# Performance work log

Hardware: AMD Instinct MI355X
Metric: run time of the kernel (lower is better)

The kernel has to match this reference:

```python
import jax, jax.numpy as jnp
import numpy as np

HEADS = 4
DIM_HEAD = 32
GROUPS = 32  # min(256//4, 32)
EPS = 1e-5


def setup_inputs() -> dict:
    key = jax.random.key(0)
    ks = jax.random.split(key, 6)
    B, C, H, W = 16, 256, 64, 64
    hidden = HEADS * DIM_HEAD  # 128
    return {
        "x": jax.random.normal(ks[0], (B, C, H, W), dtype=jnp.float32),
        "gn_w": jax.random.uniform(ks[1], (C,), dtype=jnp.float32),
        "gn_b": jax.random.normal(ks[2], (C,), dtype=jnp.float32) * 0.05,
        "qkv_w": jax.random.normal(ks[3], (3 * hidden, C), dtype=jnp.float32) * 0.05,
        "qkv_b": jax.random.normal(ks[4], (3 * hidden,), dtype=jnp.float32) * 0.05,
        "out_w": jax.random.normal(ks[5], (C, hidden), dtype=jnp.float32) * 0.05,
        "out_b": jnp.zeros((C,), dtype=jnp.float32),
    }


def _forward_single(x, gn_w, gn_b, qkv_w, qkv_b, out_w, out_b):
    # x: (c, h, w)
    c, h, w = x.shape
    # GroupNorm over (channels-in-group, h, w)
    xg = x.reshape(GROUPS, c // GROUPS, h, w)
    mean = xg.mean(axis=(1, 2, 3), keepdims=True)
    var = xg.var(axis=(1, 2, 3), keepdims=True)
    xn = ((xg - mean) * jax.lax.rsqrt(var + EPS)).reshape(c, h, w)
    xn = xn * gn_w[:, None, None] + gn_b[:, None, None]
    # 1x1 conv QKV projection
    qkv = jnp.einsum('oc,chw->ohw', qkv_w, xn) + qkv_b[:, None, None]
    qkv = qkv.reshape(3, HEADS, DIM_HEAD, h * w)
    q, k, v = qkv[0], qkv[1], qkv[2]
    k = jax.nn.softmax(k, axis=-1)  # softmax over spatial
    context = jnp.einsum('hdn,hen->hde', k, v)   # (heads, d, d)
    out = jnp.einsum('hde,hdn->hen', context, q)  # (heads, d, n)
    out = out.reshape(HEADS * DIM_HEAD, h, w)
    # 1x1 conv output projection
    return jnp.einsum('oc,chw->ohw', out_w, out) + out_b[:, None, None]


def reference(x, gn_w, gn_b, qkv_w, qkv_b, out_w, out_b):
    f = lambda xi: _forward_single(xi, gn_w, gn_b, qkv_w, qkv_b, out_w, out_b)
    return jax.vmap(f)(x)
```

## Files before the change

kernel.cpp:

```cpp
#include <hip/hip_runtime.h>
#include <stdint.h>

typedef unsigned short u16;
typedef __attribute__((ext_vector_type(8))) short bf16x8;
typedef __attribute__((ext_vector_type(4))) float f32x4;

#define B_   16
#define C_   256
#define HW_  4096
#define QR_  384
#define HID_ 128

__device__ __forceinline__ float b2f(u16 u) {
  union { uint32_t i; float f; } v; v.i = ((uint32_t)u) << 16; return v.f;
}
__device__ __forceinline__ u16 f2b(float f) {
  union { float f; uint32_t i; } v; v.f = f;
  uint32_t r = (v.i + 0x7FFFu + ((v.i >> 16) & 1u)) >> 16;
  return (u16)r;
}

__global__ __launch_bounds__(256) void gn_stats_conv_kernel(
    const float* __restrict__ x, const float* __restrict__ gnw,
    const float* __restrict__ gnb, float* __restrict__ scale,
    float* __restrict__ shiftv,
    const float* __restrict__ qkvw, u16* __restrict__ cqkvw,
    u16* __restrict__ wqT, unsigned int* __restrict__ cnt,
    float* __restrict__ ctxs)
{
  if (blockIdx.x >= 512) {
    int bi = blockIdx.x - 512;
    int t = threadIdx.x;
    if (bi < 96) {
      int i = bi * 256 + t;
      float4 f = ((const float4*)qkvw)[i];
      ushort4 o;
      o.x = f2b(f.x); o.y = f2b(f.y); o.z = f2b(f.z); o.w = f2b(f.w);
      ((ushort4*)cqkvw)[i] = o;
      return;
    }
    if (bi >= 97) {
      int z = (bi - 97) * 256 + t;
      ((float4*)ctxs)[z] = make_float4(0.f, 0.f, 0.f, 0.f);
      return;
    }
    if (t < 16) cnt[t] = 0;
    __shared__ u16 tl[16][272];
    for (int j = 0; j < 8; ++j) {
      int d = j * 16 + (t >> 4);
      int cb = (t & 15) * 16;
#pragma unroll
      for (int ii = 0; ii < 16; ++ii)
        tl[t >> 4][cb + ii] = f2b(qkvw[(size_t)d * 256 + cb + ii]);
      __syncthreads();
      union { u16 v[16]; uint4 q[2]; } pk;
#pragma unroll
      for (int dd = 0; dd < 16; ++dd) pk.v[dd] = tl[dd][t];
      *(uint4*)(wqT + (size_t)t * 128 + j * 16)     = pk.q[0];
      *(uint4*)(wqT + (size_t)t * 128 + j * 16 + 8) = pk.q[1];
      __syncthreads();
    }
    return;
  }
  int b = blockIdx.x >> 5, g = blockIdx.x & 31;
  const float* p = x + ((size_t)b * C_ + g * 8) * HW_;
  int t = threadIdx.x;
  float s = 0.f, sq = 0.f;
#pragma unroll
  for (int i = 0; i < 16; ++i) {
    float4 u0 = *(const float4*)(p + t * 8 + i * 2048);
    float4 u1 = *(const float4*)(p + t * 8 + i * 2048 + 4);
    s  += u0.x + u0.y + u0.z + u0.w + u1.x + u1.y + u1.z + u1.w;
    sq += u0.x*u0.x + u0.y*u0.y + u0.z*u0.z + u0.w*u0.w
        + u1.x*u1.x + u1.y*u1.y + u1.z*u1.z + u1.w*u1.w;
  }
#pragma unroll
  for (int off = 32; off > 0; off >>= 1) {
    s  += __shfl_down(s, off);
    sq += __shfl_down(sq, off);
  }
  __shared__ float ps[4], pq[4], mr[2];
  int lane = t & 63, w = t >> 6;
  if (lane == 0) { ps[w] = s; pq[w] = sq; }
  __syncthreads();
  if (t == 0) {
    float S = ps[0] + ps[1] + ps[2] + ps[3];
    float Q = pq[0] + pq[1] + pq[2] + pq[3];
    float mean = S * (1.f / 32768.f);
    float var  = Q * (1.f / 32768.f) - mean * mean;
    mr[0] = mean; mr[1] = rsqrtf(var + 1e-5f);
  }
  __syncthreads();
  if (t < 8) {
    int c = g * 8 + t;
    float sc = gnw[c] * mr[1];
    scale[b * C_ + c]  = sc;
    shiftv[b * C_ + c] = gnb[c] - mr[0] * sc;
  }
}

__global__ __launch_bounds__(256) void gn_transpose_kernel(
    const float* __restrict__ x, u16* __restrict__ dst,
    const float* __restrict__ scale, const float* __restrict__ shiftv)
{
  int nt = blockIdx.x, ct = blockIdx.y, b = blockIdx.z;
  const float* S = x + (size_t)b * C_ * HW_;
  u16* D = dst + (size_t)b * HW_ * C_;
  __shared__ __align__(16) u16 tile[64][136];
  int t = threadIdx.x;
  int n0 = nt * 128, c0 = ct * 64;
  int r = t >> 2, seg = (t & 3) * 32;
  float sc = scale[(size_t)b * C_ + c0 + r];
  float sh = shiftv[(size_t)b * C_ + c0 + r];
#pragma unroll
  for (int i = 0; i < 4; ++i) {
    const float* rp = S + (size_t)(c0 + r) * HW_ + n0 + seg + i * 8;
    float4 u0 = *(const float4*)(rp);
    float4 u1 = *(const float4*)(rp + 4);
    float f[8] = {u0.x, u0.y, u0.z, u0.w, u1.x, u1.y, u1.z, u1.w};
    uint4 o;
    uint32_t* op = (uint32_t*)&o;
#pragma unroll
    for (int j = 0; j < 4; ++j) {
      op[j] = (uint32_t)f2b(f[2 * j] * sc + sh)
            | ((uint32_t)f2b(f[2 * j + 1] * sc + sh) << 16);
    }
    *(uint4*)&tile[r][seg + i * 8] = o;
  }
  __syncthreads();
#pragma unroll
  for (int i = 0; i < 4; ++i) {
    int m = t * 4 + i;
    int n_l = m >> 3, cg = (m & 7) * 8;
    union { u16 v[8]; uint4 q; } pk;
#pragma unroll
    for (int e = 0; e < 8; ++e) pk.v[e] = tile[cg + e][n_l];
    *(uint4*)(D + (size_t)(n0 + n_l) * C_ + c0 + cg) = pk.q;
  }
}

__global__ __launch_bounds__(512) void kv_ctx_kernel(
    const u16* __restrict__ A,
    const u16* __restrict__ Bt,
    float* __restrict__ ctx,
    float* __restrict__ sv)
{
  const int K = C_;
  int nt = blockIdx.x, b = blockIdx.y;
  const u16* Ab = A;
  const u16* Bb = Bt + (size_t)b * HW_ * C_ + (size_t)nt * 128 * K;
  __shared__ __align__(16) union {
    struct { u16 lA[256 * 64]; u16 lB[128 * 64]; } st;
    struct { u16 ek[128][136]; u16 vv[128][136]; float sred[2][128]; } ep;
    float cred[4096];
  } sm;
  int t = threadIdx.x;
  int lane = t & 63, w = t >> 6;
  int quad = lane >> 4, l16 = lane & 15;
  int wm = (w >> 1) * 64, wn = (w & 1) * 64;
  f32x4 acc[4][4];
#pragma unroll
  for (int i = 0; i < 4; ++i)
#pragma unroll
    for (int j = 0; j < 4; ++j)
#pragma unroll
      for (int r = 0; r < 4; ++r) acc[i][j][r] = 0.f;

  for (int k0 = 0; k0 < K; k0 += 64) {
    __syncthreads();
#pragma unroll
    for (int q = 0; q < 4; ++q) {
      int ch = q * 512 + t;
      int row = ch >> 3, off = (ch & 7) * 8;
      __builtin_amdgcn_global_load_lds(
          (const __attribute__((address_space(1))) void*)(Ab + (size_t)row * K + k0 + off),
          (__attribute__((address_space(3))) void*)(sm.st.lA + ch * 8), 16, 0, 0);
    }
#pragma unroll
    for (int q = 0; q < 2; ++q) {
      int ch = q * 512 + t;
      int row = ch >> 3, off = (ch & 7) * 8;
      __builtin_amdgcn_global_load_lds(
          (const __attribute__((address_space(1))) void*)(Bb + (size_t)row * K + k0 + off),
          (__attribute__((address_space(3))) void*)(sm.st.lB + ch * 8), 16, 0, 0);
    }
    __syncthreads();
    const bf16x8* A8 = (const bf16x8*)sm.st.lA;
    const bf16x8* B8 = (const bf16x8*)sm.st.lB;
#pragma unroll
    for (int kk = 0; kk < 2; ++kk) {
      bf16x8 af[4], bfr[4];
#pragma unroll
      for (int i = 0; i < 4; ++i) af[i]  = A8[(wm + i * 16 + l16) * 8 + kk * 4 + quad];
#pragma unroll
      for (int j = 0; j < 4; ++j) bfr[j] = B8[(wn + j * 16 + l16) * 8 + kk * 4 + quad];
#pragma unroll
      for (int i = 0; i < 4; ++i)
#pragma unroll
        for (int j = 0; j < 4; ++j)
          acc[i][j] = __builtin_amdgcn_mfma_f32_16x16x32_bf16(af[i], bfr[j],
                                                              acc[i][j], 0, 0, 0);
    }
  }

  __syncthreads();
  int h = w >> 1, nh = w & 1;
  if (w < 4) {
    float sl[4][4];
#pragma unroll
    for (int i = 0; i < 4; ++i)
#pragma unroll
      for (int r = 0; r < 4; ++r) sl[i][r] = 0.f;
#pragma unroll
    for (int i = 0; i < 4; ++i)
#pragma unroll
      for (int j = 0; j < 4; ++j)
#pragma unroll
        for (int r = 0; r < 4; ++r) {
          float e = __expf(acc[i][j][r]);
          sl[i][r] += e;
          sm.ep.ek[wm + i * 16 + quad * 4 + r][wn + j * 16 + l16] = f2b(e);
        }
#pragma unroll
    for (int i = 0; i < 4; ++i)
#pragma unroll
      for (int r = 0; r < 4; ++r) {
        float v = sl[i][r];
        v += __shfl_xor(v, 1);
        v += __shfl_xor(v, 2);
        v += __shfl_xor(v, 4);
        v += __shfl_xor(v, 8);
        if (l16 == 0) sm.ep.sred[nh][wm + i * 16 + quad * 4 + r] = v;
      }
  } else {
#pragma unroll
    for (int i = 0; i < 4; ++i)
#pragma unroll
      for (int j = 0; j < 4; ++j)
#pragma unroll
        for (int r = 0; r < 4; ++r)
          sm.ep.vv[wm - 128 + i * 16 + quad * 4 + r][wn + j * 16 + l16] =
              f2b(acc[i][j][r]);
  }
  __syncthreads();
  if (t < 128)
    atomicAdd(&sv[(size_t)b * 128 + t], sm.ep.sred[0][t] + sm.ep.sred[1][t]);

  f32x4 c2[2][2];
#pragma unroll
  for (int i = 0; i < 2; ++i)
#pragma unroll
    for (int j = 0; j < 2; ++j)
#pragma unroll
      for (int r = 0; r < 4; ++r) c2[i][j][r] = 0.f;
#pragma unroll
  for (int kk = 0; kk < 2; ++kk) {
    bf16x8 ae[2], be[2];
#pragma unroll
    for (int i = 0; i < 2; ++i)
      ae[i] = *(const bf16x8*)&sm.ep.ek[h * 32 + i * 16 + l16][nh * 64 + kk * 32 + quad * 8];
#pragma unroll
    for (int j = 0; j < 2; ++j)
      be[j] = *(const bf16x8*)&sm.ep.vv[h * 32 + j * 16 + l16][nh * 64 + kk * 32 + quad * 8];
#pragma unroll
    for (int i = 0; i < 2; ++i)
#pragma unroll
      for (int j = 0; j < 2; ++j)
        c2[i][j] = __builtin_amdgcn_mfma_f32_16x16x32_bf16(ae[i], be[j], c2[i][j], 0, 0, 0);
  }
  __syncthreads();
  if (nh == 0) {
#pragma unroll
    for (int i = 0; i < 2; ++i)
#pragma unroll
      for (int j = 0; j < 2; ++j)
#pragma unroll
        for (int r = 0; r < 4; ++r)
          sm.cred[h * 1024 + (i * 16 + quad * 4 + r) * 32 + j * 16 + l16] = c2[i][j][r];
  }
  __syncthreads();
  if (nh == 1) {
#pragma unroll
    for (int i = 0; i < 2; ++i)
#pragma unroll
      for (int j = 0; j < 2; ++j)
#pragma unroll
        for (int r = 0; r < 4; ++r)
          sm.cred[h * 1024 + (i * 16 + quad * 4 + r) * 32 + j * 16 + l16] += c2[i][j][r];
  }
  __syncthreads();
  float* ctxb = ctx + (size_t)b * 4096;
#pragma unroll
  for (int u = 0; u < 8; ++u)
    atomicAdd(&ctxb[t + u * 512], sm.cred[t + u * 512]);
}

__global__ __launch_bounds__(256) void foldwtot_kernel(
    const float* __restrict__ ctx, const float* __restrict__ sv,
    const float* __restrict__ outw, const float* __restrict__ qkvb,
    const u16* __restrict__ wqT, const float* __restrict__ outb,
    u16* __restrict__ wf, u16* __restrict__ wtot,
    float* __restrict__ btot, unsigned int* __restrict__ cnt)
{
  int b = blockIdx.x >> 2, h = blockIdx.x & 3;
  int t = threadIdx.x;
  __shared__ float cs[1024];
  __shared__ float sinv[32];
  __shared__ unsigned int oldc;
  __shared__ __align__(16) u16 wfl[256 * 136];
  *(float4*)&cs[t * 4] = *(const float4*)(ctx + ((size_t)b * 4 + h) * 1024 + t * 4);
  if (t < 32) sinv[t] = 1.f / sv[(size_t)b * 128 + h * 32 + t];
  __syncthreads();
  {
    int o = t;
    const float* wr = outw + (size_t)o * HID_ + h * 32;
    float wv[32];
    float cb = 0.f;
#pragma unroll
    for (int e = 0; e < 32; ++e) {
      wv[e] = wr[e];
      cb += wv[e] * qkvb[256 + h * 32 + e];
    }
    union { u16 v[32]; uint4 q[4]; } pk;
#pragma unroll
    for (int d = 0; d < 32; ++d) {
      float a = 0.f;
#pragma unroll
      for (int e = 0; e < 32; ++e) a += wv[e] * cs[d * 32 + e];
      pk.v[d] = f2b(a * sinv[d] + cb);
    }
    uint4* dp = (uint4*)(wf + ((size_t)b * C_ + o) * HID_ + h * 32);
#pragma unroll
    for (int i = 0; i < 4; ++i) dp[i] = pk.q[i];
  }

  __threadfence();
  __syncthreads();
  if (t == 0) oldc = atomicAdd(&cnt[b], 1u);
  __syncthreads();
  if (oldc != 3) return;
  __threadfence();

  const uint4* ws4 = (const uint4*)(wf + (size_t)b * C_ * HID_);
  for (int i = t; i < 4096; i += 256) {
    uint4 v = ws4[i];
    int o_ = i >> 4, off = (i & 15) * 8;
    *(uint4*)&wfl[o_ * 136 + off] = v;
  }
  __syncthreads();
  {
    float a = outb[t];
#pragma unroll
    for (int d = 0; d < 128; ++d) a += b2f(wfl[t * 136 + d]) * qkvb[d];
    btot[(size_t)b * C_ + t] = a;
  }
  int lane = t & 63, w = t >> 6;
  int quad = lane >> 4, l16 = lane & 15;
  u16* Wb = wtot + (size_t)b * C_ * C_;
  for (int j = 0; j < 16; ++j) {
    f32x4 a4[4];
#pragma unroll
    for (int i = 0; i < 4; ++i)
#pragma unroll
      for (int r = 0; r < 4; ++r) a4[i][r] = 0.f;
#pragma unroll
    for (int kk = 0; kk < 4; ++kk) {
      bf16x8 bfj = *(const bf16x8*)(wqT + (size_t)(j * 16 + l16) * 128 + kk * 32 + quad * 8);
#pragma unroll
      for (int i = 0; i < 4; ++i) {
        bf16x8 afi = *(const bf16x8*)&wfl[(w * 64 + i * 16 + l16) * 136 + kk * 32 + quad * 8];
        a4[i] = __builtin_amdgcn_mfma_f32_16x16x32_bf16(bfj, afi, a4[i], 0, 0, 0);
      }
    }
#pragma unroll
    for (int i = 0; i < 4; ++i) {
      int oo = w * 64 + i * 16 + l16;
      int c0 = j * 16 + quad * 4;
      uint2 p2;
      p2.x = (uint32_t)f2b(a4[i][0]) | ((uint32_t)f2b(a4[i][1]) << 16);
      p2.y = (uint32_t)f2b(a4[i][2]) | ((uint32_t)f2b(a4[i][3]) << 16);
      *(uint2*)(Wb + (size_t)oo * C_ + c0) = p2;
    }
  }
}

__global__ __launch_bounds__(256) void out_gemm_kernel(
    const u16* __restrict__ wtot, const u16* __restrict__ Bt,
    const float* __restrict__ btot, float* __restrict__ Cout)
{
  const int K = C_;
  int nt = blockIdx.x, mt = blockIdx.y, b = blockIdx.z;
  const u16* Ab = wtot + (size_t)b * C_ * C_ + (size_t)mt * 128 * K;
  const u16* Bb = Bt + (size_t)b * HW_ * C_ + (size_t)nt * 128 * K;
  __shared__ __align__(16) u16 lA[128 * 64];
  __shared__ __align__(16) u16 lB[128 * 64];
  int t = threadIdx.x;
  int lane = t & 63, w = t >> 6;
  int quad = lane >> 4, l16 = lane & 15;
  int wm = (w >> 1) * 64, wn = (w & 1) * 64;
  f32x4 acc[4][4];
#pragma unroll
  for (int j = 0; j < 4; ++j)
#pragma unroll
    for (int i = 0; i < 4; ++i)
#pragma unroll
      for (int r = 0; r < 4; ++r) acc[j][i][r] = 0.f;

  for (int k0 = 0; k0 < K; k0 += 64) {
    __syncthreads();
#pragma unroll
    for (int q = 0; q < 4; ++q) {
      int ch = q * 256 + t;
      int row = ch >> 3, off = (ch & 7) * 8;
      __builtin_amdgcn_global_load_lds(
          (const __attribute__((address_space(1))) void*)(Ab + (size_t)row * K + k0 + off),
          (__attribute__((address_space(3))) void*)(lA + ch * 8), 16, 0, 0);
      __builtin_amdgcn_global_load_lds(
          (const __attribute__((address_space(1))) void*)(Bb + (size_t)row * K + k0 + off),
          (__attribute__((address_space(3))) void*)(lB + ch * 8), 16, 0, 0);
    }
    __syncthreads();
    const bf16x8* A8 = (const bf16x8*)lA;
    const bf16x8* B8 = (const bf16x8*)lB;
#pragma unroll
    for (int kk = 0; kk < 2; ++kk) {
      bf16x8 af[4], bfr[4];
#pragma unroll
      for (int i = 0; i < 4; ++i) af[i]  = A8[(wm + i * 16 + l16) * 8 + kk * 4 + quad];
#pragma unroll
      for (int j = 0; j < 4; ++j) bfr[j] = B8[(wn + j * 16 + l16) * 8 + kk * 4 + quad];
#pragma unroll
      for (int j = 0; j < 4; ++j)
#pragma unroll
        for (int i = 0; i < 4; ++i)
          acc[j][i] = __builtin_amdgcn_mfma_f32_16x16x32_bf16(bfr[j], af[i],
                                                              acc[j][i], 0, 0, 0);
    }
  }
#pragma unroll
  for (int i = 0; i < 4; ++i) {
    int o = mt * 128 + wm + i * 16 + l16;
    float bo = btot[(size_t)b * C_ + o];
    size_t rowbase = (size_t)b * C_ * HW_ + (size_t)o * HW_;
#pragma unroll
    for (int j = 0; j < 4; ++j) {
      int n0 = nt * 128 + wn + j * 16 + quad * 4;
      float4 v = make_float4(acc[j][i][0] + bo, acc[j][i][1] + bo,
                             acc[j][i][2] + bo, acc[j][i][3] + bo);
      *(float4*)(Cout + rowbase + n0) = v;
    }
  }
}

extern "C" void kernel_launch(void* const* d_in, const int* in_sizes, int n_in,
                              void* d_out, int out_size, void* d_ws, size_t ws_size,
                              hipStream_t stream)
{
  const float* x    = (const float*)d_in[0];
  const float* gnw  = (const float*)d_in[1];
  const float* gnb  = (const float*)d_in[2];
  const float* qkvw = (const float*)d_in[3];
  const float* qkvb = (const float*)d_in[4];
  const float* outw = (const float*)d_in[5];
  const float* outb = (const float*)d_in[6];

  char* p = (char*)d_ws;
  float* scale  = (float*)p;            p += (size_t)B_ * C_ * 4;
  float* shiftv = (float*)p;            p += (size_t)B_ * C_ * 4;
  u16* cqkvw = (u16*)p;                 p += (size_t)QR_ * C_ * 2;
  u16* wqT   = (u16*)p;                 p += (size_t)C_ * HID_ * 2;
  u16* xn_t  = (u16*)p;                 p += (size_t)B_ * HW_ * C_ * 2;
  u16* wf    = (u16*)p;                 p += (size_t)B_ * C_ * HID_ * 2;
  u16* wtot  = (u16*)p;                 p += (size_t)B_ * C_ * C_ * 2;
  float* ctxs = (float*)p;              p += (size_t)67584 * 4;
  float* btot = (float*)p;              p += (size_t)B_ * C_ * 4;
  unsigned int* cnt = (unsigned int*)p; p += 16 * 4;
  float* ctx = ctxs;
  float* sv  = ctxs + 65536;

  gn_stats_conv_kernel<<<675, 256, 0, stream>>>(x, gnw, gnb, scale, shiftv,
                                                qkvw, cqkvw, wqT, cnt, ctxs);
  gn_transpose_kernel<<<dim3(32, 4, 16), 256, 0, stream>>>(x, xn_t, scale, shiftv);
  kv_ctx_kernel<<<dim3(32, 16), 512, 0, stream>>>(cqkvw + 128 * C_, xn_t, ctx, sv);
  foldwtot_kernel<<<64, 256, 0, stream>>>(ctx, sv, outw, qkvb, wqT, outb,
                                          wf, wtot, btot, cnt);
  out_gemm_kernel<<<dim3(32, 2, 16), 256, 0, stream>>>(wtot, xn_t, btot,
                                                       (float*)d_out);
}
```

Baseline: 223.3 us.

## Merge per-head fold blocks into one block per batch, drop atomic counter handoff

The fold kernel used to launch four blocks per batch, one per head. Each wrote its slice of the folded weight to global memory, and the last block to arrive, detected through an atomic counter, finished the Wtot GEMM. Now a single block per batch computes all four heads into shared memory and runs the GEMM directly. This removes the global round-trip, the threadfences and the counter reset. In exchange the launch drops from 64 blocks to 16, so there is less parallelism in the head-fold phase.

Result: slower. 232.7 us (+4.2%).

```diff
diff --git a/kernel.cpp b/kernel.cpp
--- a/kernel.cpp
+++ b/kernel.cpp
@@ -25,8 +25,7 @@
     const float* __restrict__ gnb, float* __restrict__ scale,
     float* __restrict__ shiftv,
     const float* __restrict__ qkvw, u16* __restrict__ cqkvw,
-    u16* __restrict__ wqT, unsigned int* __restrict__ cnt,
-    float* __restrict__ ctxs)
+    u16* __restrict__ wqT, float* __restrict__ ctxs)
 {
   if (blockIdx.x >= 512) {
     int bi = blockIdx.x - 512;
@@ -44,7 +43,6 @@
       ((float4*)ctxs)[z] = make_float4(0.f, 0.f, 0.f, 0.f);
       return;
     }
-    if (t < 16) cnt[t] = 0;
     __shared__ u16 tl[16][272];
     for (int j = 0; j < 8; ++j) {
       int d = j * 16 + (t >> 4);
@@ -299,61 +297,59 @@
     const float* __restrict__ ctx, const float* __restrict__ sv,
     const float* __restrict__ outw, const float* __restrict__ qkvb,
     const u16* __restrict__ wqT, const float* __restrict__ outb,
-    u16* __restrict__ wf, u16* __restrict__ wtot,
-    float* __restrict__ btot, unsigned int* __restrict__ cnt)
-{
-  int b = blockIdx.x >> 2, h = blockIdx.x & 3;
+    u16* __restrict__ wtot, float* __restrict__ btot)
+{
+  int b = blockIdx.x;
   int t = threadIdx.x;
-  __shared__ float cs[1024];
-  __shared__ float sinv[32];
-  __shared__ unsigned int oldc;
+  __shared__ float cs[4096];
+  __shared__ float sinv[128];
   __shared__ __align__(16) u16 wfl[256 * 136];
-  *(float4*)&cs[t * 4] = *(const float4*)(ctx + ((size_t)b * 4 + h) * 1024 + t * 4);
-  if (t < 32) sinv[t] = 1.f / sv[(size_t)b * 128 + h * 32 + t];
-  __syncthreads();
+  const float4* cp = (const float4*)(ctx + (size_t)b * 4096);
+  float4* cs4 = (float4*)cs;
+#pragma unroll
+  for (int i = 0; i < 4; ++i) cs4[t + i * 256] = cp[t + i * 256];
+  if (t < 128) sinv[t] = 1.f / sv[(size_t)b * 128 + t];
+  __syncthreads();
+
   {
     int o = t;
-    const float* wr = outw + (size_t)o * HID_ + h * 32;
-    float wv[32];
-    float cb = 0.f;
-#pragma unroll
-    for (int e = 0; e < 32; ++e) {
-      wv[e] = wr[e];
-      cb += wv[e] * qkvb[256 + h * 32 + e];
-    }
-    union { u16 v[32]; uint4 q[4]; } pk;
-#pragma unroll
-    for (int d = 0; d < 32; ++d) {
-      float a = 0.f;
-#pragma unroll
-      for (int e = 0; e < 32; ++e) a += wv[e] * cs[d * 32 + e];
-      pk.v[d] = f2b(a * sinv[d] + cb);
-    }
-    uint4* dp = (uint4*)(wf + ((size_t)b * C_ + o) * HID_ + h * 32);
-#pragma unroll
-    for (int i = 0; i < 4; ++i) dp[i] = pk.q[i];
-  }
-
-  __threadfence();
-  __syncthreads();
-  if (t == 0) oldc = atomicAdd(&cnt[b], 1u);
-  __syncthreads();
-  if (oldc != 3) return;
-  __threadfence();
-
-  const uint4* ws4 = (const uint4*)(wf + (size_t)b * C_ * HID_);
-  for (int i = t; i < 4096; i += 256) {
-    uint4 v = ws4[i];
-    int o_ = i >> 4, off = (i & 15) * 8;
-    *(uint4*)&wfl[o_ * 136 + off] = v;
-  }
-  __syncthreads();
+#pragma unroll
+    for (int h = 0; h < 4; ++h) {
+      const float* wr = outw + (size_t)o * HID_ + h * 32;
+      float wv[32];
+      float cb = 0.f;
+#pragma unroll
+      for (int e = 0; e < 32; ++e) {
+        wv[e] = wr[e];
+        cb += wv[e] * qkvb[256 + h * 32 + e];
+      }
+      union { u16 v[32]; uint4 q[4]; } pk;
+#pragma unroll
+      for (int d = 0; d < 32; ++d) {
+        float a = 0.f;
+#pragma unroll
+        for (int e = 0; e < 32; ++e) a += wv[e] * cs[h * 1024 + d * 32 + e];
+        pk.v[d] = f2b(a * sinv[h * 32 + d] + cb);
+      }
+#pragma unroll
+      for (int i = 0; i < 4; ++i)
+        *(uint4*)&wfl[o * 136 + h * 32 + i * 8] = pk.q[i];
+    }
+  }
+  __syncthreads();
+
   {
     float a = outb[t];
 #pragma unroll
-    for (int d = 0; d < 128; ++d) a += b2f(wfl[t * 136 + d]) * qkvb[d];
+    for (int i = 0; i < 16; ++i) {
+      union { uint4 q; u16 v[8]; } u;
+      u.q = *(const uint4*)&wfl[t * 136 + i * 8];
+#pragma unroll
+      for (int e = 0; e < 8; ++e) a += b2f(u.v[e]) * qkvb[i * 8 + e];
+    }
     btot[(size_t)b * C_ + t] = a;
   }
+
   int lane = t & 63, w = t >> 6;
   int quad = lane >> 4, l16 = lane & 15;
   u16* Wb = wtot + (size_t)b * C_ * C_;
@@ -470,20 +466,18 @@
   u16* cqkvw = (u16*)p;                 p += (size_t)QR_ * C_ * 2;
   u16* wqT   = (u16*)p;                 p += (size_t)C_ * HID_ * 2;
   u16* xn_t  = (u16*)p;                 p += (size_t)B_ * HW_ * C_ * 2;
-  u16* wf    = (u16*)p;                 p += (size_t)B_ * C_ * HID_ * 2;
   u16* wtot  = (u16*)p;                 p += (size_t)B_ * C_ * C_ * 2;
   float* ctxs = (float*)p;              p += (size_t)67584 * 4;
-  float* btot = (float*)p;              p += (size_t)B_ * C_ * 4;
-  unsigned int* cnt = (unsigned int*)p; p += 16 * 4;
+  float* btot = (float*)p;
   float* ctx = ctxs;
   float* sv  = ctxs + 65536;
 
   gn_stats_conv_kernel<<<675, 256, 0, stream>>>(x, gnw, gnb, scale, shiftv,
-                                                qkvw, cqkvw, wqT, cnt, ctxs);
+                                                qkvw, cqkvw, wqT, ctxs);
   gn_transpose_kernel<<<dim3(32, 4, 16), 256, 0, stream>>>(x, xn_t, scale, shiftv);
   kv_ctx_kernel<<<dim3(32, 16), 512, 0, stream>>>(cqkvw + 128 * C_, xn_t, ctx, sv);
-  foldwtot_kernel<<<64, 256, 0, stream>>>(ctx, sv, outw, qkvb, wqT, outb,
-                                          wf, wtot, btot, cnt);
+  foldwtot_kernel<<<16, 256, 0, stream>>>(ctx, sv, outw, qkvb, wqT, outb,
+                                          wtot, btot);
   out_gemm_kernel<<<dim3(32, 2, 16), 256, 0, stream>>>(wtot, xn_t, btot,
                                                        (float*)d_out);
 }
```
